# Optimization experiments

Hardware: AMD Instinct MI355X
Metric: run time of the kernel (lower is better)

Reference implementation:

```python
import jax, jax.numpy as jnp
import numpy as np

ALPHA = 0.5  # smooth_quant migration strength
N_TOKENS, D_MODEL = 32768, 1024  # square linear: d_in == d_out (required by diag_s @ weight)


def setup_inputs() -> dict:
    key = jax.random.key(0)
    k1, k2, k3 = jax.random.split(key, 3)
    x = jax.random.normal(k1, (N_TOKENS, D_MODEL), dtype=jnp.float32)
    weight = jax.random.normal(k2, (D_MODEL, D_MODEL), dtype=jnp.float32) * 0.02
    bias = jax.random.normal(k3, (D_MODEL,), dtype=jnp.float32) * 0.02
    return {"x": x, "weight": weight, "bias": bias}


def reference(x, weight, bias):
    # SmoothQuant rescale: per-in-channel maxima of activations and weight.
    max_act = jnp.max(x, axis=0) ** ALPHA                 # [D]
    max_w = jnp.max(weight, axis=0) ** (1.0 - ALPHA)      # [D] (max over out dim -> per in-channel)
    s = max_act / max_w                                   # [D] scale_fact
    # x_hat = x @ diag(s)^-1 ; expressed as the equivalent per-channel broadcast.
    x_hat = x / s                                         # [N, D]
    # weight_hat = diag(s) @ weight (square linear, row rescale).
    w_hat = s[:, None] * weight                           # [D, D]
    # nn.Linear forward: x_hat @ weight_hat^T + bias
    return x_hat @ w_hat.T + bias
```

## Files before the change

kernel.cpp:

```cpp
#include <hip/hip_runtime.h>
#include <hip/hip_bf16.h>
#include <stdint.h>

#define D_MODEL 1024
#define BM 128
#define BN 128
#define BK 64

typedef __attribute__((ext_vector_type(4))) float  f32x4;
typedef __attribute__((ext_vector_type(8))) __bf16 bf16x8;
typedef __attribute__((ext_vector_type(8))) unsigned short u16x8;
typedef __attribute__((ext_vector_type(4))) unsigned short u16x4;


__device__ __forceinline__ unsigned order_map(float x) {
    unsigned u = __float_as_uint(x);
    return (u & 0x80000000u) ? ~u : (u | 0x80000000u);
}
__device__ __forceinline__ float order_unmap(unsigned m) {
    unsigned b = (m & 0x80000000u) ? (m & 0x7fffffffu) : ~m;
    return __uint_as_float(b);
}
__device__ __forceinline__ unsigned short f2bf(float f) {
    unsigned u = __float_as_uint(f);
    u += 0x7fffu + ((u >> 16) & 1u);
    return (unsigned short)(u >> 16);
}


__global__ void init_u32(unsigned* __restrict__ p, int n) {
    int i = blockIdx.x * blockDim.x + threadIdx.x;
    if (i < n) p[i] = 0u;
}

__global__ void colmax_kernel(const float* __restrict__ src, int rows_per_slab,
                              int cols, unsigned* __restrict__ out_u) {
    int k = blockIdx.x * blockDim.x + threadIdx.x;
    const float* p = src + (size_t)blockIdx.y * rows_per_slab * cols + k;
    float m = -__builtin_inff();
#pragma unroll 4
    for (int r = 0; r < rows_per_slab; ++r)
        m = fmaxf(m, p[(size_t)r * cols]);
    atomicMax(&out_u[k], order_map(m));
}

#define CC_ROWS 16
__global__ __launch_bounds__(256)
void colmax_convert(const float* __restrict__ x,
                    float* __restrict__ partial,
                    unsigned short* __restrict__ xb) {
    int c4 = threadIdx.x * 4;
    size_t base = (size_t)blockIdx.x * CC_ROWS * D_MODEL + c4;
    f32x4 m4 = {-__builtin_inff(), -__builtin_inff(), -__builtin_inff(), -__builtin_inff()};
#pragma unroll 8
    for (int r = 0; r < CC_ROWS; ++r) {
        f32x4 v = *reinterpret_cast<const f32x4*>(&x[base + (size_t)r * D_MODEL]);
        u16x4 o;
#pragma unroll
        for (int e = 0; e < 4; ++e) { m4[e] = fmaxf(m4[e], v[e]); o[e] = f2bf(v[e]); }
        *reinterpret_cast<u16x4*>(&xb[base + (size_t)r * D_MODEL]) = o;
    }
    *reinterpret_cast<f32x4*>(&partial[(size_t)blockIdx.x * D_MODEL + c4]) = m4;
}

__global__ void reduce_partial(const float* __restrict__ partial,
                               unsigned* __restrict__ ma_u) {
    int col  = blockIdx.x * 256 + threadIdx.x;
    int b0   = blockIdx.y * 64;
    float m = -__builtin_inff();
#pragma unroll 8
    for (int i = 0; i < 64; ++i)
        m = fmaxf(m, partial[(size_t)(b0 + i) * D_MODEL + col]);
    atomicMax(&ma_u[col], order_map(m));
}

__global__ void scale_kernel(const unsigned* __restrict__ ma_u,
                             const unsigned* __restrict__ mw_u,
                             float* __restrict__ s) {
    int k = blockIdx.x * blockDim.x + threadIdx.x;
    if (k < D_MODEL) {
        float ma = order_unmap(ma_u[k]);
        float mw = order_unmap(mw_u[k]);
        s[k] = sqrtf(ma) / sqrtf(mw);
    }
}

__global__ void build_w_kernel(const float* __restrict__ W, const float* __restrict__ s,
                               unsigned short* __restrict__ Wp) {
    int j  = blockIdx.x;
    int k4 = threadIdx.x * 4;
    float sj = s[j];
    f32x4 w  = *reinterpret_cast<const f32x4*>(&W[(size_t)j * D_MODEL + k4]);
    f32x4 sk = *reinterpret_cast<const f32x4*>(&s[k4]);
    u16x4 o;
#pragma unroll
    for (int i = 0; i < 4; ++i) o[i] = f2bf(sj * w[i] / sk[i]);
    *reinterpret_cast<u16x4*>(&Wp[(size_t)j * D_MODEL + k4]) = o;
}

__global__ __launch_bounds__(256)
void gemm_db(const unsigned short* __restrict__ Xb,
             const unsigned short* __restrict__ Wp, const float* __restrict__ bias,
             float* __restrict__ out, int N) {
    __shared__ __align__(16) unsigned short As[2][BM][BK];
    __shared__ __align__(16) unsigned short Bs[2][BN][BK];

    int flat = blockIdx.x;
    int swz  = ((gridDim.x & 7) == 0)
             ? (flat & 7) * (gridDim.x >> 3) + (flat >> 3)
             : flat;
    const int nColBlk = D_MODEL / BN;
    int row0 = (swz / nColBlk) * BM;
    int col0 = (swz % nColBlk) * BN;

    int tid  = threadIdx.x;
    int wave = tid >> 6;
    int lane = tid & 63;
    int wr   = wave >> 1;
    int wc   = wave & 1;
    int l16  = lane & 15;

    int srow  = lane >> 3;
    int skoff = ((lane & 7) ^ srow) << 3;

    f32x4 acc[4][4];
#pragma unroll
    for (int m = 0; m < 4; ++m)
#pragma unroll
        for (int n = 0; n < 4; ++n)
            acc[m][n] = (f32x4){0.f, 0.f, 0.f, 0.f};

    const int NT = D_MODEL / BK;

    auto stage = [&](int t, int b) {
        int k0 = t * BK;
#pragma unroll
        for (int i = 0; i < 4; ++i) {
            int r0 = (wave * 4 + i) * 8;
            const unsigned short* gA = Xb + (size_t)(row0 + r0 + srow) * D_MODEL + k0 + skoff;
            __builtin_amdgcn_global_load_lds(
                (const __attribute__((address_space(1))) void*)gA,
                (__attribute__((address_space(3))) void*)&As[b][r0][0], 16, 0, 0);
            const unsigned short* gB = Wp + (size_t)(col0 + r0 + srow) * D_MODEL + k0 + skoff;
            __builtin_amdgcn_global_load_lds(
                (const __attribute__((address_space(1))) void*)gB,
                (__attribute__((address_space(3))) void*)&Bs[b][r0][0], 16, 0, 0);
        }
    };

    stage(0, 0);
    asm volatile("s_waitcnt vmcnt(0)" ::: "memory");
    __builtin_amdgcn_s_barrier();

    for (int t = 0; t < NT; ++t) {
        int cur = t & 1;
        if (t + 1 < NT) stage(t + 1, cur ^ 1);

        const char* Ab = (const char*)&As[cur][0][0];
        const char* Bb = (const char*)&Bs[cur][0][0];
#pragma unroll
        for (int kk = 0; kk < 2; ++kk) {
            bf16x8 af[4], bf_[4];
#pragma unroll
            for (int m = 0; m < 4; ++m) {
                int row = wr * 64 + m * 16 + l16;
                int o   = ((lane >> 4) * 16 + kk * 64) ^ ((row & 7) << 4);
                af[m] = *reinterpret_cast<const bf16x8*>(Ab + row * 128 + o);
            }
#pragma unroll
            for (int n = 0; n < 4; ++n) {
                int row = wc * 64 + n * 16 + l16;
                int o   = ((lane >> 4) * 16 + kk * 64) ^ ((row & 7) << 4);
                bf_[n] = *reinterpret_cast<const bf16x8*>(Bb + row * 128 + o);
            }
#pragma unroll
            for (int m = 0; m < 4; ++m)
#pragma unroll
                for (int n = 0; n < 4; ++n)
                    acc[m][n] = __builtin_amdgcn_mfma_f32_16x16x32_bf16(
                        af[m], bf_[n], acc[m][n], 0, 0, 0);
        }

        if (t + 1 < NT) {
            asm volatile("s_waitcnt vmcnt(0)" ::: "memory");
            __builtin_amdgcn_s_barrier();
        }
    }

    int crow = row0 + wr * 64;
    int ccol = col0 + wc * 64;
#pragma unroll
    for (int n = 0; n < 4; ++n) {
        int col = ccol + n * 16 + l16;
        float b = bias[col];
#pragma unroll
        for (int m = 0; m < 4; ++m) {
            int r = crow + m * 16 + (lane >> 4) * 4;
#pragma unroll
            for (int q = 0; q < 4; ++q)
                out[(size_t)(r + q) * D_MODEL + col] = acc[m][n][q] + b;
        }
    }
}

__global__ __launch_bounds__(256)
void gemm_fallback(const float* __restrict__ X, const unsigned short* __restrict__ Wp,
                   const float* __restrict__ bias, float* __restrict__ out, int N) {
    __shared__ __align__(16) unsigned short As[BM][BK];
    __shared__ __align__(16) unsigned short Bs[BN][BK];

    int flat = blockIdx.x;
    int swz  = ((gridDim.x & 7) == 0)
             ? (flat & 7) * (gridDim.x >> 3) + (flat >> 3) : flat;
    const int nColBlk = D_MODEL / BN;
    int row0 = (swz / nColBlk) * BM;
    int col0 = (swz % nColBlk) * BN;

    int tid  = threadIdx.x;
    int wave = tid >> 6;
    int lane = tid & 63;
    int wr   = wave >> 1;
    int wc   = wave & 1;
    int l16  = lane & 15;
    int srow  = lane >> 3;
    int skoff = ((lane & 7) ^ srow) << 3;

    f32x4 acc[4][4];
#pragma unroll
    for (int m = 0; m < 4; ++m)
#pragma unroll
        for (int n = 0; n < 4; ++n)
            acc[m][n] = (f32x4){0.f, 0.f, 0.f, 0.f};

    for (int k0 = 0; k0 < D_MODEL; k0 += BK) {
        __syncthreads();
#pragma unroll
        for (int i = 0; i < 4; ++i) {
            int c   = i * 256 + tid;
            int r   = c >> 3;
            int seg = c & 7;
            const float* gp = X + (size_t)(row0 + r) * D_MODEL + k0 + seg * 8;
            f32x4 x0 = *reinterpret_cast<const f32x4*>(gp);
            f32x4 x1 = *reinterpret_cast<const f32x4*>(gp + 4);
            u16x8 v;
#pragma unroll
            for (int e = 0; e < 4; ++e) { v[e] = f2bf(x0[e]); v[e + 4] = f2bf(x1[e]); }
            int off = (seg * 16) ^ ((r & 7) << 4);
            *reinterpret_cast<u16x8*>((char*)&As[0][0] + r * 128 + off) = v;
        }
#pragma unroll
        for (int i = 0; i < 4; ++i) {
            int r0 = (wave * 4 + i) * 8;
            const unsigned short* g = Wp + (size_t)(col0 + r0 + srow) * D_MODEL + k0 + skoff;
            __builtin_amdgcn_global_load_lds(
                (const __attribute__((address_space(1))) void*)g,
                (__attribute__((address_space(3))) void*)&Bs[r0][0], 16, 0, 0);
        }
        __syncthreads();
#pragma unroll
        for (int kk = 0; kk < 2; ++kk) {
            bf16x8 af[4], bf_[4];
#pragma unroll
            for (int m = 0; m < 4; ++m) {
                int row = wr * 64 + m * 16 + l16;
                int o   = ((lane >> 4) * 16 + kk * 64) ^ ((row & 7) << 4);
                af[m] = *reinterpret_cast<const bf16x8*>((const char*)&As[0][0] + row * 128 + o);
            }
#pragma unroll
            for (int n = 0; n < 4; ++n) {
                int row = wc * 64 + n * 16 + l16;
                int o   = ((lane >> 4) * 16 + kk * 64) ^ ((row & 7) << 4);
                bf_[n] = *reinterpret_cast<const bf16x8*>((const char*)&Bs[0][0] + row * 128 + o);
            }
#pragma unroll
            for (int m = 0; m < 4; ++m)
#pragma unroll
                for (int n = 0; n < 4; ++n)
                    acc[m][n] = __builtin_amdgcn_mfma_f32_16x16x32_bf16(
                        af[m], bf_[n], acc[m][n], 0, 0, 0);
        }
    }

    int crow = row0 + wr * 64;
    int ccol = col0 + wc * 64;
#pragma unroll
    for (int n = 0; n < 4; ++n) {
        int col = ccol + n * 16 + l16;
        float b = bias[col];
#pragma unroll
        for (int m = 0; m < 4; ++m) {
            int r = crow + m * 16 + (lane >> 4) * 4;
#pragma unroll
            for (int q = 0; q < 4; ++q)
                out[(size_t)(r + q) * D_MODEL + col] = acc[m][n][q] + b;
        }
    }
}


extern "C" void kernel_launch(void* const* d_in, const int* in_sizes, int n_in,
                              void* d_out, int out_size, void* d_ws, size_t ws_size,
                              hipStream_t stream) {
    const float* x    = (const float*)d_in[0];
    const float* w    = (const float*)d_in[1];
    const float* bias = (const float*)d_in[2];
    float* out        = (float*)d_out;
    const int N       = in_sizes[0] / D_MODEL;

    char* ws               = (char*)d_ws;
    unsigned*       ma_u   = (unsigned*)(ws);
    unsigned*       mw_u   = (unsigned*)(ws + 4096);
    float*          s      = (float*)(ws + 8192);
    unsigned short* Wp     = (unsigned short*)(ws + 16384);
    unsigned short* Xb     = (unsigned short*)(ws + 16384 + (size_t)D_MODEL * D_MODEL * 2);
    const int nPart        = N / CC_ROWS;
    float*          part   = (float*)(ws + 16384 + (size_t)D_MODEL * D_MODEL * 2
                                               + (size_t)N * D_MODEL * 2);

    size_t need = 16384 + (size_t)D_MODEL * D_MODEL * 2 + (size_t)N * D_MODEL * 2
                + (size_t)nPart * D_MODEL * 4;
    bool preconv = ws_size >= need;

    init_u32<<<8, 256, 0, stream>>>((unsigned*)ws, 2048);

    if (preconv) {
        colmax_convert<<<nPart, 256, 0, stream>>>(x, part, Xb);
        reduce_partial<<<dim3(D_MODEL / 256, nPart / 64), 256, 0, stream>>>(part, ma_u);
    } else {
        colmax_kernel<<<dim3(D_MODEL / 256, 64), 256, 0, stream>>>(x, N / 64, D_MODEL, ma_u);
    }
    colmax_kernel<<<dim3(D_MODEL / 256, 16), 256, 0, stream>>>(w, D_MODEL / 16, D_MODEL, mw_u);
    scale_kernel<<<D_MODEL / 256, 256, 0, stream>>>(ma_u, mw_u, s);
    build_w_kernel<<<D_MODEL, 256, 0, stream>>>(w, s, Wp);

    int nblk = (N / BM) * (D_MODEL / BN);
    if (preconv)
        gemm_db<<<nblk, 256, 0, stream>>>(Xb, Wp, bias, out, N);
    else
        gemm_fallback<<<nblk, 256, 0, stream>>>(x, Wp, bias, out, N);
}
```

Measured before the change: 161.8 us.

## Replace GEMM with 256x256 eight-wave kernel using phased prefetch and setprio

Replaces the 128x128, 4-wave double-buffered bf16 GEMM with a 256x256 tile, 512-thread kernel. Each k-step is split into four quadrant phases separated by barriers, with the next tile's A and B global-to-LDS loads issued between phases and s_setprio raised around MFMA bursts. The larger tile improves operand reuse from LDS and the phasing is meant to overlap loads with MFMA work. In exchange it uses 128KB of LDS per block, adds many barriers, and increases register pressure from the 64 accumulators per wave.

```diff
diff --git a/kernel.cpp b/kernel.cpp
--- a/kernel.cpp
+++ b/kernel.cpp
@@ -3,9 +3,6 @@
 #include <stdint.h>
 
 #define D_MODEL 1024
-#define BM 128
-#define BN 128
-#define BK 64
 
 typedef __attribute__((ext_vector_type(4))) float  f32x4;
 typedef __attribute__((ext_vector_type(8))) __bf16 bf16x8;
@@ -98,123 +95,179 @@
     *reinterpret_cast<u16x4*>(&Wp[(size_t)j * D_MODEL + k4]) = o;
 }
 
-__global__ __launch_bounds__(256)
-void gemm_db(const unsigned short* __restrict__ Xb,
-             const unsigned short* __restrict__ Wp, const float* __restrict__ bias,
-             float* __restrict__ out, int N) {
-    __shared__ __align__(16) unsigned short As[2][BM][BK];
-    __shared__ __align__(16) unsigned short Bs[2][BN][BK];
+#define GBM 256
+#define GBN 256
+#define GBK 64
+#define GNT (D_MODEL / GBK)
+
+__global__ __launch_bounds__(512, 2)
+void gemm_8ph(const unsigned short* __restrict__ Xb,
+              const unsigned short* __restrict__ Wp,
+              const float* __restrict__ bias,
+              float* __restrict__ out) {
+    __shared__ __align__(16) unsigned short As[2][GBM][GBK];
+    __shared__ __align__(16) unsigned short Bs[2][GBN][GBK];
 
     int flat = blockIdx.x;
-    int swz  = ((gridDim.x & 7) == 0)
-             ? (flat & 7) * (gridDim.x >> 3) + (flat >> 3)
-             : flat;
-    const int nColBlk = D_MODEL / BN;
-    int row0 = (swz / nColBlk) * BM;
-    int col0 = (swz % nColBlk) * BN;
+    int swz  = (flat & 7) * (gridDim.x >> 3) + (flat >> 3);
+    const int nRowBlk = 32768 / GBM;
+    int row0 = (swz % nRowBlk) * GBM;
+    int col0 = (swz / nRowBlk) * GBN;
 
     int tid  = threadIdx.x;
     int wave = tid >> 6;
     int lane = tid & 63;
-    int wr   = wave >> 1;
-    int wc   = wave & 1;
+    int wr   = wave >> 2;
+    int wc   = wave & 3;
     int l16  = lane & 15;
-
+    int lq   = lane >> 4;
     int srow  = lane >> 3;
     int skoff = ((lane & 7) ^ srow) << 3;
 
-    f32x4 acc[4][4];
-#pragma unroll
-    for (int m = 0; m < 4; ++m)
-#pragma unroll
-        for (int n = 0; n < 4; ++n)
-            acc[m][n] = (f32x4){0.f, 0.f, 0.f, 0.f};
-
-    const int NT = D_MODEL / BK;
-
-    auto stage = [&](int t, int b) {
-        int k0 = t * BK;
+    f32x4 acc[2][2][4][2];
+#pragma unroll
+    for (int mq = 0; mq < 2; ++mq)
+#pragma unroll
+        for (int nq = 0; nq < 2; ++nq)
+#pragma unroll
+            for (int m = 0; m < 4; ++m)
+#pragma unroll
+                for (int n = 0; n < 2; ++n)
+                    acc[mq][nq][m][n] = (f32x4){0.f, 0.f, 0.f, 0.f};
+
+    auto stageA = [&](int t, int b) {
+        int k0 = t * GBK;
 #pragma unroll
         for (int i = 0; i < 4; ++i) {
-            int r0 = (wave * 4 + i) * 8;
-            const unsigned short* gA = Xb + (size_t)(row0 + r0 + srow) * D_MODEL + k0 + skoff;
+            int rg = wave * 4 + i;
+            const unsigned short* g = Xb + (size_t)(row0 + rg * 8 + srow) * D_MODEL + k0 + skoff;
             __builtin_amdgcn_global_load_lds(
-                (const __attribute__((address_space(1))) void*)gA,
-                (__attribute__((address_space(3))) void*)&As[b][r0][0], 16, 0, 0);
-            const unsigned short* gB = Wp + (size_t)(col0 + r0 + srow) * D_MODEL + k0 + skoff;
+                (const __attribute__((address_space(1))) void*)g,
+                (__attribute__((address_space(3))) void*)&As[b][rg * 8][0], 16, 0, 0);
+        }
+    };
+    auto stageB = [&](int t, int b) {
+        int k0 = t * GBK;
+#pragma unroll
+        for (int i = 0; i < 4; ++i) {
+            int rg = wave * 4 + i;
+            const unsigned short* g = Wp + (size_t)(col0 + rg * 8 + srow) * D_MODEL + k0 + skoff;
             __builtin_amdgcn_global_load_lds(
-                (const __attribute__((address_space(1))) void*)gB,
-                (__attribute__((address_space(3))) void*)&Bs[b][r0][0], 16, 0, 0);
+                (const __attribute__((address_space(1))) void*)g,
+                (__attribute__((address_space(3))) void*)&Bs[b][rg * 8][0], 16, 0, 0);
         }
     };
 
-    stage(0, 0);
+    stageA(0, 0); stageB(0, 0);
     asm volatile("s_waitcnt vmcnt(0)" ::: "memory");
     __builtin_amdgcn_s_barrier();
 
-    for (int t = 0; t < NT; ++t) {
+#pragma unroll 1
+    for (int t = 0; t < GNT; ++t) {
         int cur = t & 1;
-        if (t + 1 < NT) stage(t + 1, cur ^ 1);
-
         const char* Ab = (const char*)&As[cur][0][0];
         const char* Bb = (const char*)&Bs[cur][0][0];
-#pragma unroll
-        for (int kk = 0; kk < 2; ++kk) {
-            bf16x8 af[4], bf_[4];
-#pragma unroll
-            for (int m = 0; m < 4; ++m) {
-                int row = wr * 64 + m * 16 + l16;
-                int o   = ((lane >> 4) * 16 + kk * 64) ^ ((row & 7) << 4);
-                af[m] = *reinterpret_cast<const bf16x8*>(Ab + row * 128 + o);
-            }
-#pragma unroll
-            for (int n = 0; n < 4; ++n) {
-                int row = wc * 64 + n * 16 + l16;
-                int o   = ((lane >> 4) * 16 + kk * 64) ^ ((row & 7) << 4);
-                bf_[n] = *reinterpret_cast<const bf16x8*>(Bb + row * 128 + o);
-            }
+        bool pf = (t < GNT - 1);
+
+        bf16x8 af[4][2], bf[2][2];
+
+        auto lda = [&](int mq, int m, int kk) {
+            int row  = wr * 128 + mq * 64 + m * 16 + l16;
+            int slot = (kk * 4 + lq) ^ (row & 7);
+            return *reinterpret_cast<const bf16x8*>(Ab + row * 128 + slot * 16);
+        };
+        auto ldb = [&](int nq, int n, int kk) {
+            int row  = wc * 64 + nq * 32 + n * 16 + l16;
+            int slot = (kk * 4 + lq) ^ (row & 7);
+            return *reinterpret_cast<const bf16x8*>(Bb + row * 128 + slot * 16);
+        };
+        auto quad = [&](int mq, int nq) {
+            __builtin_amdgcn_s_setprio(1);
 #pragma unroll
             for (int m = 0; m < 4; ++m)
 #pragma unroll
-                for (int n = 0; n < 4; ++n)
-                    acc[m][n] = __builtin_amdgcn_mfma_f32_16x16x32_bf16(
-                        af[m], bf_[n], acc[m][n], 0, 0, 0);
-        }
-
-        if (t + 1 < NT) {
+                for (int n = 0; n < 2; ++n)
+#pragma unroll
+                    for (int kk = 0; kk < 2; ++kk)
+                        acc[mq][nq][m][n] = __builtin_amdgcn_mfma_f32_16x16x32_bf16(
+                            af[m][kk], bf[n][kk], acc[mq][nq][m][n], 0, 0, 0);
+            __builtin_amdgcn_s_setprio(0);
+        };
+
+#pragma unroll
+        for (int m = 0; m < 4; ++m)
+#pragma unroll
+            for (int kk = 0; kk < 2; ++kk) af[m][kk] = lda(0, m, kk);
+#pragma unroll
+        for (int n = 0; n < 2; ++n)
+#pragma unroll
+            for (int kk = 0; kk < 2; ++kk) bf[n][kk] = ldb(0, n, kk);
+        if (pf) stageA(t + 1, cur ^ 1);
+        __builtin_amdgcn_s_barrier();
+        quad(0, 0);
+        __builtin_amdgcn_s_barrier();
+
+#pragma unroll
+        for (int n = 0; n < 2; ++n)
+#pragma unroll
+            for (int kk = 0; kk < 2; ++kk) bf[n][kk] = ldb(1, n, kk);
+        if (pf) stageB(t + 1, cur ^ 1);
+        __builtin_amdgcn_s_barrier();
+        quad(0, 1);
+        __builtin_amdgcn_s_barrier();
+
+#pragma unroll
+        for (int m = 0; m < 4; ++m)
+#pragma unroll
+            for (int kk = 0; kk < 2; ++kk) af[m][kk] = lda(1, m, kk);
+        __builtin_amdgcn_s_barrier();
+        quad(1, 1);
+        __builtin_amdgcn_s_barrier();
+
+#pragma unroll
+        for (int n = 0; n < 2; ++n)
+#pragma unroll
+            for (int kk = 0; kk < 2; ++kk) bf[n][kk] = ldb(0, n, kk);
+        __builtin_amdgcn_s_barrier();
+        quad(1, 0);
+        if (pf) {
             asm volatile("s_waitcnt vmcnt(0)" ::: "memory");
             __builtin_amdgcn_s_barrier();
         }
     }
 
-    int crow = row0 + wr * 64;
+    int crow = row0 + wr * 128;
     int ccol = col0 + wc * 64;
 #pragma unroll
-    for (int n = 0; n < 4; ++n) {
-        int col = ccol + n * 16 + l16;
-        float b = bias[col];
-#pragma unroll
-        for (int m = 0; m < 4; ++m) {
-            int r = crow + m * 16 + (lane >> 4) * 4;
-#pragma unroll
-            for (int q = 0; q < 4; ++q)
-                out[(size_t)(r + q) * D_MODEL + col] = acc[m][n][q] + b;
-        }
-    }
+    for (int nq = 0; nq < 2; ++nq)
+#pragma unroll
+        for (int n = 0; n < 2; ++n) {
+            int col = ccol + nq * 32 + n * 16 + l16;
+            float b = bias[col];
+#pragma unroll
+            for (int mq = 0; mq < 2; ++mq)
+#pragma unroll
+                for (int m = 0; m < 4; ++m) {
+                    int r = crow + mq * 64 + m * 16 + lq * 4;
+#pragma unroll
+                    for (int q = 0; q < 4; ++q)
+                        out[(size_t)(r + q) * D_MODEL + col] = acc[mq][nq][m][n][q] + b;
+                }
+        }
 }
 
 __global__ __launch_bounds__(256)
 void gemm_fallback(const float* __restrict__ X, const unsigned short* __restrict__ Wp,
                    const float* __restrict__ bias, float* __restrict__ out, int N) {
-    __shared__ __align__(16) unsigned short As[BM][BK];
-    __shared__ __align__(16) unsigned short Bs[BN][BK];
+    __shared__ __align__(16) unsigned short As[128][64];
+    __shared__ __align__(16) unsigned short Bs[128][64];
 
     int flat = blockIdx.x;
     int swz  = ((gridDim.x & 7) == 0)
              ? (flat & 7) * (gridDim.x >> 3) + (flat >> 3) : flat;
-    const int nColBlk = D_MODEL / BN;
-    int row0 = (swz / nColBlk) * BM;
-    int col0 = (swz % nColBlk) * BN;
+    const int nColBlk = D_MODEL / 128;
+    int row0 = (swz / nColBlk) * 128;
+    int col0 = (swz % nColBlk) * 128;
 
     int tid  = threadIdx.x;
     int wave = tid >> 6;
@@ -232,7 +285,7 @@
         for (int n = 0; n < 4; ++n)
             acc[m][n] = (f32x4){0.f, 0.f, 0.f, 0.f};
 
-    for (int k0 = 0; k0 < D_MODEL; k0 += BK) {
+    for (int k0 = 0; k0 < D_MODEL; k0 += 64) {
         __syncthreads();
 #pragma unroll
         for (int i = 0; i < 4; ++i) {
@@ -333,9 +386,11 @@
     scale_kernel<<<D_MODEL / 256, 256, 0, stream>>>(ma_u, mw_u, s);
     build_w_kernel<<<D_MODEL, 256, 0, stream>>>(w, s, Wp);
 
-    int nblk = (N / BM) * (D_MODEL / BN);
-    if (preconv)
-        gemm_db<<<nblk, 256, 0, stream>>>(Xb, Wp, bias, out, N);
-    else
+    if (preconv) {
+        int nblk = (N / GBM) * (D_MODEL / GBN);
+        gemm_8ph<<<nblk, 512, 0, stream>>>(Xb, Wp, bias, out);
+    } else {
+        int nblk = (N / 128) * (D_MODEL / 128);
         gemm_fallback<<<nblk, 256, 0, stream>>>(x, Wp, bias, out, N);
-}
+    }
+}
```

Measured after the change: 170.8 us. 5.6% more time.

## Replace GEMM with 256x256 tile, 8-wave, triple-buffered LDS pipeline

Applied to the files above, without the earlier changes.

Replaces the 128x128x64 double-buffered bf16 GEMM with a 256x256x32 tile run by 512 threads. It uses three LDS buffers, so loads are issued two stages ahead with a partial vmcnt wait. The block-to-tile mapping assigns rows per XCD so the chiplets share data better. MFMA sections are wrapped in setprio. The larger tile halves global traffic per FLOP, at the cost of more accumulator registers per wave and fewer blocks, which could hurt occupancy.

```diff
diff --git a/kernel.cpp b/kernel.cpp
--- a/kernel.cpp
+++ b/kernel.cpp
@@ -3,9 +3,6 @@
 #include <stdint.h>
 
 #define D_MODEL 1024
-#define BM 128
-#define BN 128
-#define BK 64
 
 typedef __attribute__((ext_vector_type(4))) float  f32x4;
 typedef __attribute__((ext_vector_type(8))) __bf16 bf16x8;
@@ -98,104 +95,121 @@
     *reinterpret_cast<u16x4*>(&Wp[(size_t)j * D_MODEL + k4]) = o;
 }
 
-__global__ __launch_bounds__(256)
-void gemm_db(const unsigned short* __restrict__ Xb,
-             const unsigned short* __restrict__ Wp, const float* __restrict__ bias,
-             float* __restrict__ out, int N) {
-    __shared__ __align__(16) unsigned short As[2][BM][BK];
-    __shared__ __align__(16) unsigned short Bs[2][BN][BK];
-
-    int flat = blockIdx.x;
-    int swz  = ((gridDim.x & 7) == 0)
-             ? (flat & 7) * (gridDim.x >> 3) + (flat >> 3)
-             : flat;
-    const int nColBlk = D_MODEL / BN;
-    int row0 = (swz / nColBlk) * BM;
-    int col0 = (swz % nColBlk) * BN;
+#define GBM 256
+#define GBN 256
+#define GBK 32
+#define GNT (D_MODEL / GBK)
+#define BUF_SHORTS 8192
+
+__global__ __launch_bounds__(512, 2)
+void gemm_main(const unsigned short* __restrict__ Xb,
+               const unsigned short* __restrict__ Wp,
+               const float* __restrict__ bias,
+               float* __restrict__ out) {
+    __shared__ __align__(16) unsigned short lds[6 * BUF_SHORTS];
+
+    int flat  = blockIdx.x;
+    int xcd   = flat & 7;
+    int j     = flat >> 3;
+    int col0  = (j & 3) * GBN;
+    int row0  = ((xcd << 4) + (j >> 2)) * GBM;
 
     int tid  = threadIdx.x;
     int wave = tid >> 6;
     int lane = tid & 63;
-    int wr   = wave >> 1;
-    int wc   = wave & 1;
+    int wr   = wave >> 2;
+    int wc   = wave & 3;
     int l16  = lane & 15;
-
-    int srow  = lane >> 3;
-    int skoff = ((lane & 7) ^ srow) << 3;
-
-    f32x4 acc[4][4];
-#pragma unroll
-    for (int m = 0; m < 4; ++m)
+    int lq   = lane >> 4;
+
+    int sline = lane >> 3;
+    int slog  = (lane & 7) ^ sline;
+    int sh    = slog >> 2;
+    int sq    = slog & 3;
+
+    f32x4 acc[8][4];
+#pragma unroll
+    for (int m = 0; m < 8; ++m)
 #pragma unroll
         for (int n = 0; n < 4; ++n)
             acc[m][n] = (f32x4){0.f, 0.f, 0.f, 0.f};
 
-    const int NT = D_MODEL / BK;
-
     auto stage = [&](int t, int b) {
-        int k0 = t * BK;
-#pragma unroll
-        for (int i = 0; i < 4; ++i) {
-            int r0 = (wave * 4 + i) * 8;
-            const unsigned short* gA = Xb + (size_t)(row0 + r0 + srow) * D_MODEL + k0 + skoff;
+        int k0 = t * GBK;
+#pragma unroll
+        for (int r = 0; r < 2; ++r) {
+            int line = r * 64 + wave * 8 + sline;
+            const unsigned short* gA =
+                Xb + (size_t)(row0 + 2 * line + sh) * D_MODEL + k0 + sq * 8;
             __builtin_amdgcn_global_load_lds(
                 (const __attribute__((address_space(1))) void*)gA,
-                (__attribute__((address_space(3))) void*)&As[b][r0][0], 16, 0, 0);
-            const unsigned short* gB = Wp + (size_t)(col0 + r0 + srow) * D_MODEL + k0 + skoff;
+                (__attribute__((address_space(3))) void*)&lds[b * BUF_SHORTS + line * 64],
+                16, 0, 0);
+            const unsigned short* gB =
+                Wp + (size_t)(col0 + 2 * line + sh) * D_MODEL + k0 + sq * 8;
             __builtin_amdgcn_global_load_lds(
                 (const __attribute__((address_space(1))) void*)gB,
-                (__attribute__((address_space(3))) void*)&Bs[b][r0][0], 16, 0, 0);
+                (__attribute__((address_space(3))) void*)&lds[(3 + b) * BUF_SHORTS + line * 64],
+                16, 0, 0);
         }
     };
 
     stage(0, 0);
-    asm volatile("s_waitcnt vmcnt(0)" ::: "memory");
-    __builtin_amdgcn_s_barrier();
-
-    for (int t = 0; t < NT; ++t) {
-        int cur = t & 1;
-        if (t + 1 < NT) stage(t + 1, cur ^ 1);
-
-        const char* Ab = (const char*)&As[cur][0][0];
-        const char* Bb = (const char*)&Bs[cur][0][0];
-#pragma unroll
-        for (int kk = 0; kk < 2; ++kk) {
-            bf16x8 af[4], bf_[4];
-#pragma unroll
-            for (int m = 0; m < 4; ++m) {
-                int row = wr * 64 + m * 16 + l16;
-                int o   = ((lane >> 4) * 16 + kk * 64) ^ ((row & 7) << 4);
-                af[m] = *reinterpret_cast<const bf16x8*>(Ab + row * 128 + o);
-            }
-#pragma unroll
-            for (int n = 0; n < 4; ++n) {
-                int row = wc * 64 + n * 16 + l16;
-                int o   = ((lane >> 4) * 16 + kk * 64) ^ ((row & 7) << 4);
-                bf_[n] = *reinterpret_cast<const bf16x8*>(Bb + row * 128 + o);
-            }
-#pragma unroll
-            for (int m = 0; m < 4; ++m)
-#pragma unroll
-                for (int n = 0; n < 4; ++n)
-                    acc[m][n] = __builtin_amdgcn_mfma_f32_16x16x32_bf16(
-                        af[m], bf_[n], acc[m][n], 0, 0, 0);
-        }
-
-        if (t + 1 < NT) {
-            asm volatile("s_waitcnt vmcnt(0)" ::: "memory");
-            __builtin_amdgcn_s_barrier();
-        }
-    }
-
-    int crow = row0 + wr * 64;
+    stage(1, 1);
+
+    int cur = 0;
+#pragma unroll 1
+    for (int t = 0; t < GNT; ++t) {
+        if (t + 1 < GNT) asm volatile("s_waitcnt vmcnt(4)" ::: "memory");
+        else             asm volatile("s_waitcnt vmcnt(0)" ::: "memory");
+        __builtin_amdgcn_s_barrier();
+
+        if (t + 2 < GNT) {
+            int bnext = cur >= 1 ? cur - 1 : cur + 2;
+            stage(t + 2, bnext);
+        }
+
+        const char* Ab = (const char*)&lds[cur * BUF_SHORTS];
+        const char* Bb = (const char*)&lds[(3 + cur) * BUF_SHORTS];
+
+        bf16x8 bfr[4];
+#pragma unroll
+        for (int n = 0; n < 4; ++n) {
+            int cc   = wc * 64 + n * 16 + l16;
+            int line = cc >> 1;
+            int o    = (((cc & 1) << 6) + (lq << 4)) ^ ((line & 7) << 4);
+            bfr[n] = *reinterpret_cast<const bf16x8*>(Bb + line * 128 + o);
+        }
+        bf16x8 afr[8];
+#pragma unroll
+        for (int m = 0; m < 8; ++m) {
+            int rr   = wr * 128 + m * 16 + l16;
+            int line = rr >> 1;
+            int o    = (((rr & 1) << 6) + (lq << 4)) ^ ((line & 7) << 4);
+            afr[m] = *reinterpret_cast<const bf16x8*>(Ab + line * 128 + o);
+        }
+
+        __builtin_amdgcn_s_setprio(1);
+#pragma unroll
+        for (int m = 0; m < 8; ++m)
+#pragma unroll
+            for (int n = 0; n < 4; ++n)
+                acc[m][n] = __builtin_amdgcn_mfma_f32_16x16x32_bf16(
+                    afr[m], bfr[n], acc[m][n], 0, 0, 0);
+        __builtin_amdgcn_s_setprio(0);
+
+        cur = cur == 2 ? 0 : cur + 1;
+    }
+
+    int crow = row0 + wr * 128;
     int ccol = col0 + wc * 64;
 #pragma unroll
     for (int n = 0; n < 4; ++n) {
         int col = ccol + n * 16 + l16;
         float b = bias[col];
 #pragma unroll
-        for (int m = 0; m < 4; ++m) {
-            int r = crow + m * 16 + (lane >> 4) * 4;
+        for (int m = 0; m < 8; ++m) {
+            int r = crow + m * 16 + lq * 4;
 #pragma unroll
             for (int q = 0; q < 4; ++q)
                 out[(size_t)(r + q) * D_MODEL + col] = acc[m][n][q] + b;
@@ -206,15 +220,15 @@
 __global__ __launch_bounds__(256)
 void gemm_fallback(const float* __restrict__ X, const unsigned short* __restrict__ Wp,
                    const float* __restrict__ bias, float* __restrict__ out, int N) {
-    __shared__ __align__(16) unsigned short As[BM][BK];
-    __shared__ __align__(16) unsigned short Bs[BN][BK];
+    __shared__ __align__(16) unsigned short As[128][64];
+    __shared__ __align__(16) unsigned short Bs[128][64];
 
     int flat = blockIdx.x;
     int swz  = ((gridDim.x & 7) == 0)
              ? (flat & 7) * (gridDim.x >> 3) + (flat >> 3) : flat;
-    const int nColBlk = D_MODEL / BN;
-    int row0 = (swz / nColBlk) * BM;
-    int col0 = (swz % nColBlk) * BN;
+    const int nColBlk = D_MODEL / 128;
+    int row0 = (swz / nColBlk) * 128;
+    int col0 = (swz % nColBlk) * 128;
 
     int tid  = threadIdx.x;
     int wave = tid >> 6;
@@ -232,7 +246,7 @@
         for (int n = 0; n < 4; ++n)
             acc[m][n] = (f32x4){0.f, 0.f, 0.f, 0.f};
 
-    for (int k0 = 0; k0 < D_MODEL; k0 += BK) {
+    for (int k0 = 0; k0 < D_MODEL; k0 += 64) {
         __syncthreads();
 #pragma unroll
         for (int i = 0; i < 4; ++i) {
@@ -333,9 +347,11 @@
     scale_kernel<<<D_MODEL / 256, 256, 0, stream>>>(ma_u, mw_u, s);
     build_w_kernel<<<D_MODEL, 256, 0, stream>>>(w, s, Wp);
 
-    int nblk = (N / BM) * (D_MODEL / BN);
-    if (preconv)
-        gemm_db<<<nblk, 256, 0, stream>>>(Xb, Wp, bias, out, N);
-    else
+    if (preconv) {
+        int nblk = (N / GBM) * (D_MODEL / GBN);
+        gemm_main<<<nblk, 512, 0, stream>>>(Xb, Wp, bias, out);
+    } else {
+        int nblk = (N / 128) * (D_MODEL / 128);
         gemm_fallback<<<nblk, 256, 0, stream>>>(x, Wp, bias, out, N);
-}
+    }
+}
```

Result: faster. 154.0 us (-4.8%).
